# Kernel optimization log

Hardware: AMD Instinct MI355X
Metric: run time of the kernel (lower is better)

The kernel has to match this reference:

```python
import jax, jax.numpy as jnp
import numpy as np

NUM_ANCHORS = 5
NUM_CLASSES = 20


def setup_inputs() -> dict:
    key = jax.random.key(0)
    k1, k2, k3, k4 = jax.random.split(key, 4)
    N, H, W, M = 64, 52, 52, 32
    img = 1664
    x = jax.random.normal(k1, (N, NUM_ANCHORS * (5 + NUM_CLASSES), H, W), jnp.float32)
    anchors = jnp.array([[1.08, 1.19], [3.42, 4.41], [6.63, 11.38],
                         [9.42, 5.11], [16.62, 10.52]], jnp.float32)
    # valid gt boxes in xyxy pixel coords
    xy = jax.random.uniform(k2, (N, M, 2), jnp.float32) * (img * 0.8)
    wh = jax.random.uniform(k3, (N, M, 2), jnp.float32) * (img * 0.2) + 1.0
    gt_boxes = jnp.concatenate([xy, xy + wh], axis=-1)
    gt_labels = jax.random.randint(k4, (N, M), 0, NUM_CLASSES)
    return dict(x=x, anchors=anchors, gt_boxes=gt_boxes, gt_labels=gt_labels,
                img_h=img, img_w=img)


def _format_outputs(x, anchors, img_h, img_w):
    # x: [N, A*(5+C), H, W] -> (coords [N,HW,A,4] (x,y,w,h), obj [N,HW,A], scores [N,HW,A,C])
    N, _, H, W = x.shape
    A = anchors.shape[0]
    t = x.reshape(N, A, 5 + NUM_CLASSES, H, W).transpose(0, 3, 4, 1, 2)  # [N,H,W,A,5+C]
    c_x = jnp.arange(W, dtype=x.dtype) * (img_w / W)
    c_y = jnp.arange(H, dtype=x.dtype) * (img_h / H)
    b_x = jax.nn.sigmoid(t[..., 0]) + c_x[None, None, :, None]   # [N,H,W,A]
    b_y = jax.nn.sigmoid(t[..., 1]) + c_y[None, :, None, None]
    b_w = (img_w / W) * anchors[:, 0] * jnp.exp(t[..., 2])
    b_h = (img_h / H) * anchors[:, 1] * jnp.exp(t[..., 3])
    coords = jnp.stack([b_x, b_y, b_w, b_h], axis=-1).reshape(N, H * W, A, 4)
    b_o = jax.nn.sigmoid(t[..., 4]).reshape(N, H * W, A)
    scores = t[..., 5:].reshape(N, H * W, A, NUM_CLASSES)
    return coords, b_o, scores


def reference(x, anchors, gt_boxes, gt_labels, img_h, img_w):
    coords, b_o, scores = _format_outputs(x, anchors, img_h, img_w)
    # pred_boxes[..., 2:] += pred_boxes[..., :2]  (xywh -> xyxy)
    boxes = jnp.concatenate([coords[..., :2], coords[..., :2] + coords[..., 2:]], axis=-1)  # [N,HW,A,4]
    # box_iou: pred [N,HW,A,1,4] vs gt [N,1,1,M,4] -> [N,HW,A,M]
    p = boxes[..., None, :]
    g = gt_boxes[:, None, None, :, :]
    lt = jnp.maximum(p[..., :2], g[..., :2])
    rb = jnp.minimum(p[..., 2:], g[..., 2:])
    whi = jnp.clip(rb - lt, 0.0)
    inter = whi[..., 0] * whi[..., 1]
    area_p = (boxes[..., 2] - boxes[..., 0]) * (boxes[..., 3] - boxes[..., 1])
    area_g = (gt_boxes[..., 2] - gt_boxes[..., 0]) * (gt_boxes[..., 3] - gt_boxes[..., 1])
    iou = inter / (area_p[..., None] + area_g[:, None, None, :] - inter)   # [N,HW,A,M]

    cell_sel = iou.max(axis=(2, 3)) > 0.0                 # [N,HW]
    best_a = jnp.argmax(iou.max(axis=3), axis=2)          # [N,HW] best anchor per cell
    iou_best = jnp.take_along_axis(iou, best_a[..., None, None], axis=2)[:, :, 0, :]  # [N,HW,M]
    max_iou = iou_best.max(axis=-1)                       # [N,HW]
    gt_idx = jnp.argmax(iou_best, axis=-1)                # [N,HW]

    sel_box = jnp.take_along_axis(boxes, best_a[..., None, None], axis=2)[:, :, 0, :]   # [N,HW,4]
    sel_o = jnp.take_along_axis(b_o, best_a[..., None], axis=2)[:, :, 0]                # [N,HW]
    sel_sc = jnp.take_along_axis(scores, best_a[..., None, None], axis=2)[:, :, 0, :]   # [N,HW,C]
    g_box = jnp.take_along_axis(gt_boxes, gt_idx[..., None], axis=1)                    # [N,HW,4]
    g_lab = jnp.take_along_axis(gt_labels, gt_idx, axis=1)                              # [N,HW]

    m = cell_sel.astype(x.dtype)
    objectness_loss = (jnp.sum(m * (sel_o - max_iou) ** 2)
                       + 0.5 * jnp.sum((1.0 - m) * b_o.max(axis=2) ** 2))
    bbox_loss = (jnp.sum(m * jnp.sum((sel_box[..., :2] - g_box[..., :2]) ** 2, axis=-1))
                 + jnp.sum(m * jnp.sum((jnp.sqrt(sel_box[..., 2:]) - jnp.sqrt(g_box[..., 2:])) ** 2, axis=-1)))
    logp = jax.nn.log_softmax(sel_sc, axis=-1)
    ce = -jnp.take_along_axis(logp, g_lab[..., None], axis=-1)[..., 0]
    clf_loss = jnp.sum(m * ce)
    return jnp.stack([objectness_loss, bbox_loss, clf_loss])
```

## Files before the change

kernel.cpp:

```cpp
#include <hip/hip_runtime.h>
#include <math.h>

#define A_ 5
#define C_ 20
#define N_ 64
#define H_ 52
#define W_ 52
#define HW_ (H_ * W_)
#define M_ 32
#define CH_ (A_ * (5 + C_))
#define CPB 64
#define NBLK_X ((HW_ + CPB - 1) / CPB)
#define NBLK (NBLK_X * N_)

__global__ __launch_bounds__(320) void yolo_main(
    const float* __restrict__ x,
    const float* __restrict__ anchors,
    const float* __restrict__ gt,
    const int* __restrict__ glab,
    const void* img_h_p, const void* img_w_p,
    float* __restrict__ ws)
{
    __shared__ float s_c[8][A_][CPB];

    const int tid  = threadIdx.x;
    const int a    = tid >> 6;
    const int lane = tid & 63;
    const int n    = blockIdx.y;
    const int cell = blockIdx.x * CPB + lane;
    const bool valid = cell < HW_;

    int ibw = *(const int*)img_w_p;
    float img_w = (ibw > 0 && ibw < 1000000) ? (float)ibw : *(const float*)img_w_p;
    int ibh = *(const int*)img_h_p;
    float img_h = (ibh > 0 && ibh < 1000000) ? (float)ibh : *(const float*)img_h_p;
    const float sx = img_w / (float)W_;
    const float sy = img_h / (float)H_;

    const float ax = anchors[2 * a];
    const float ay = anchors[2 * a + 1];

    float bi = 0.f, bu = 1.f;
    int   bm = 0;
    float x1 = 0.f, y1 = 0.f, x2 = 0.f, y2 = 0.f, ov = 0.f;

    if (valid) {
        const int wi = cell % W_;
        const int hi = cell / W_;
        const size_t base = (size_t)n * CH_ * HW_ + (size_t)a * 25 * HW_ + cell;
        float t0 = x[base];
        float t1 = x[base + (size_t)HW_];
        float t2 = x[base + 2 * (size_t)HW_];
        float t3 = x[base + 3 * (size_t)HW_];
        float t4 = x[base + 4 * (size_t)HW_];

        float bx = 1.f / (1.f + __expf(-t0)) + (float)wi * sx;
        float by = 1.f / (1.f + __expf(-t1)) + (float)hi * sy;
        float bw = sx * ax * __expf(t2);
        float bh = sy * ay * __expf(t3);
        x1 = bx; y1 = by; x2 = bx + bw; y2 = by + bh;
        ov = 1.f / (1.f + __expf(-t4));
        float ap = (x2 - x1) * (y2 - y1);

        const float4* gtv = (const float4*)(gt + (size_t)n * M_ * 4);
        #pragma unroll 8
        for (int m = 0; m < M_; ++m) {
            float4 g = gtv[m];
            float area = (g.z - g.x) * (g.w - g.y);
            float wxi = fminf(x2, g.z) - fmaxf(x1, g.x);
            float hyi = fminf(y2, g.w) - fmaxf(y1, g.y);
            wxi = fmaxf(wxi, 0.f);
            hyi = fmaxf(hyi, 0.f);
            float inter = wxi * hyi;
            float uni = ap + area - inter;
            if (inter * bu > bi * uni) { bi = inter; bu = uni; bm = m; }
        }
    }

    s_c[0][a][lane] = bi;
    s_c[1][a][lane] = bu;
    s_c[2][a][lane] = x1;
    s_c[3][a][lane] = y1;
    s_c[4][a][lane] = x2;
    s_c[5][a][lane] = y2;
    s_c[6][a][lane] = ov;
    s_c[7][a][lane] = __int_as_float(bm);
    __syncthreads();

    if (tid < 64) {
        float obj = 0.f, bbx = 0.f, clf = 0.f;

        float Bi = 0.f, Bu = 1.f;
        int Ba = 0, Bm = 0;
        float X1 = 0.f, Y1 = 0.f, X2 = 0.f, Y2 = 0.f, O = 0.f;
        float bomax = -1e30f;
        #pragma unroll
        for (int aa = 0; aa < A_; ++aa) {
            float ci = s_c[0][aa][lane];
            float cu = s_c[1][aa][lane];
            float co = s_c[6][aa][lane];
            bomax = fmaxf(bomax, co);
            bool upd = (aa == 0) || (ci * Bu > Bi * cu);
            if (upd) {
                Bi = ci; Bu = cu; Ba = aa;
                Bm = __float_as_int(s_c[7][aa][lane]);
                X1 = s_c[2][aa][lane]; Y1 = s_c[3][aa][lane];
                X2 = s_c[4][aa][lane]; Y2 = s_c[5][aa][lane];
                O = co;
            }
        }

        if (valid) {
            if (Bi > 0.f) {
                float miou = Bi / Bu;
                float d = O - miou;
                obj = d * d;

                float4 g = ((const float4*)gt)[n * M_ + Bm];
                float d0 = X1 - g.x;
                float d1 = Y1 - g.y;
                float d2 = sqrtf(X2) - sqrtf(g.z);
                float d3 = sqrtf(Y2) - sqrtf(g.w);
                bbx = d0 * d0 + d1 * d1 + d2 * d2 + d3 * d3;

                const size_t sb = (size_t)n * CH_ * HW_ + (size_t)(Ba * 25 + 5) * HW_ + cell;
                const int lab = glab[n * M_ + Bm];
                float mx = -1e30f, se = 0.f, scl = 0.f;
                #pragma unroll
                for (int j = 0; j < C_; ++j) {
                    float v = x[sb + (size_t)j * HW_];
                    float nm = fmaxf(mx, v);
                    se = se * __expf(mx - nm) + __expf(v - nm);
                    mx = nm;
                    scl = (j == lab) ? v : scl;
                }
                clf = mx + __logf(se) - scl;
            } else {
                obj = 0.5f * bomax * bomax;
            }
        }

        #pragma unroll
        for (int off = 32; off > 0; off >>= 1) {
            obj += __shfl_down(obj, off, 64);
            bbx += __shfl_down(bbx, off, 64);
            clf += __shfl_down(clf, off, 64);
        }
        if (tid == 0) {
            const int bid = blockIdx.y * gridDim.x + blockIdx.x;
            ws[bid * 3 + 0] = obj;
            ws[bid * 3 + 1] = bbx;
            ws[bid * 3 + 2] = clf;
        }
    }
}

__global__ __launch_bounds__(256) void yolo_reduce(
    const float* __restrict__ ws, float* __restrict__ out)
{
    __shared__ float s_red[4][3];
    const int tid = threadIdx.x;
    float o = 0.f, b = 0.f, c = 0.f;
    for (int e = tid; e < NBLK; e += 256) {
        o += ws[e * 3 + 0];
        b += ws[e * 3 + 1];
        c += ws[e * 3 + 2];
    }
    #pragma unroll
    for (int off = 32; off > 0; off >>= 1) {
        o += __shfl_down(o, off, 64);
        b += __shfl_down(b, off, 64);
        c += __shfl_down(c, off, 64);
    }
    const int wid = tid >> 6;
    if ((tid & 63) == 0) {
        s_red[wid][0] = o; s_red[wid][1] = b; s_red[wid][2] = c;
    }
    __syncthreads();
    if (tid == 0) {
        float oo = 0.f, bb = 0.f, cc = 0.f;
        #pragma unroll
        for (int w = 0; w < 4; ++w) {
            oo += s_red[w][0]; bb += s_red[w][1]; cc += s_red[w][2];
        }
        out[0] = oo; out[1] = bb; out[2] = cc;
    }
}

extern "C" void kernel_launch(void* const* d_in, const int* in_sizes, int n_in,
                              void* d_out, int out_size, void* d_ws, size_t ws_size,
                              hipStream_t stream) {
    const float* x    = (const float*)d_in[0];
    const float* anch = (const float*)d_in[1];
    const float* gt   = (const float*)d_in[2];
    const int*   gl   = (const int*)d_in[3];
    const void*  ih   = d_in[4];
    const void*  iw   = d_in[5];
    float* out = (float*)d_out;
    float* ws  = (float*)d_ws;

    dim3 grid(NBLK_X, N_);
    yolo_main<<<grid, dim3(320), 0, stream>>>(x, anch, gt, gl, ih, iw, ws);
    yolo_reduce<<<1, 256, 0, stream>>>(ws, out);
}
```

Measured before the change: 141.7 us.

## Compute per-anchor CE and bbox loss upfront, removing dependent score gather

Each anchor thread now loads its 20 class logits together with its box channels and computes its own cross-entropy and bbox error against its best-matching gt box. The winner selection then just picks precomputed values from shared memory. This removes a serialized second read of class scores done by a single wavefront per block, at the cost of redundant softmax work on every anchor and more registers. The workspace partials are also switched to a struct-of-arrays layout and the final reduce uses 1024 threads.

```diff
diff --git a/kernel.cpp b/kernel.cpp
--- a/kernel.cpp
+++ b/kernel.cpp
@@ -21,7 +21,7 @@
     const void* img_h_p, const void* img_w_p,
     float* __restrict__ ws)
 {
-    __shared__ float s_c[8][A_][CPB];
+    __shared__ float s_c[5][A_][CPB];
 
     const int tid  = threadIdx.x;
     const int a    = tid >> 6;
@@ -42,7 +42,7 @@
 
     float bi = 0.f, bu = 1.f;
     int   bm = 0;
-    float x1 = 0.f, y1 = 0.f, x2 = 0.f, y2 = 0.f, ov = 0.f;
+    float ov = 0.f, ce = 0.f, bb = 0.f;
 
     if (valid) {
         const int wi = cell % W_;
@@ -53,12 +53,16 @@
         float t2 = x[base + 2 * (size_t)HW_];
         float t3 = x[base + 3 * (size_t)HW_];
         float t4 = x[base + 4 * (size_t)HW_];
+        float sc[C_];
+        #pragma unroll
+        for (int j = 0; j < C_; ++j)
+            sc[j] = x[base + (size_t)(5 + j) * HW_];
 
         float bx = 1.f / (1.f + __expf(-t0)) + (float)wi * sx;
         float by = 1.f / (1.f + __expf(-t1)) + (float)hi * sy;
         float bw = sx * ax * __expf(t2);
         float bh = sy * ay * __expf(t3);
-        x1 = bx; y1 = by; x2 = bx + bw; y2 = by + bh;
+        float x1 = bx, y1 = by, x2 = bx + bw, y2 = by + bh;
         ov = 1.f / (1.f + __expf(-t4));
         float ap = (x2 - x1) * (y2 - y1);
 
@@ -75,66 +79,58 @@
             float uni = ap + area - inter;
             if (inter * bu > bi * uni) { bi = inter; bu = uni; bm = m; }
         }
+
+        float4 g = ((const float4*)gt)[n * M_ + bm];
+        int lab = glab[n * M_ + bm];
+        float d0 = x1 - g.x;
+        float d1 = y1 - g.y;
+        float d2 = sqrtf(x2) - sqrtf(g.z);
+        float d3 = sqrtf(y2) - sqrtf(g.w);
+        bb = d0 * d0 + d1 * d1 + d2 * d2 + d3 * d3;
+
+        float mx = sc[0];
+        #pragma unroll
+        for (int j = 1; j < C_; ++j) mx = fmaxf(mx, sc[j]);
+        float se = 0.f, scl = sc[0];
+        #pragma unroll
+        for (int j = 0; j < C_; ++j) {
+            se += __expf(sc[j] - mx);
+            scl = (j == lab) ? sc[j] : scl;
+        }
+        ce = mx + __logf(se) - scl;
     }
 
     s_c[0][a][lane] = bi;
     s_c[1][a][lane] = bu;
-    s_c[2][a][lane] = x1;
-    s_c[3][a][lane] = y1;
-    s_c[4][a][lane] = x2;
-    s_c[5][a][lane] = y2;
-    s_c[6][a][lane] = ov;
-    s_c[7][a][lane] = __int_as_float(bm);
+    s_c[2][a][lane] = ov;
+    s_c[3][a][lane] = ce;
+    s_c[4][a][lane] = bb;
     __syncthreads();
 
     if (tid < 64) {
-        float obj = 0.f, bbx = 0.f, clf = 0.f;
-
-        float Bi = 0.f, Bu = 1.f;
-        int Ba = 0, Bm = 0;
-        float X1 = 0.f, Y1 = 0.f, X2 = 0.f, Y2 = 0.f, O = 0.f;
+        float Bi = 0.f, Bu = 1.f, O = 0.f, CE = 0.f, BB = 0.f;
         float bomax = -1e30f;
         #pragma unroll
         for (int aa = 0; aa < A_; ++aa) {
             float ci = s_c[0][aa][lane];
             float cu = s_c[1][aa][lane];
-            float co = s_c[6][aa][lane];
+            float co = s_c[2][aa][lane];
             bomax = fmaxf(bomax, co);
             bool upd = (aa == 0) || (ci * Bu > Bi * cu);
             if (upd) {
-                Bi = ci; Bu = cu; Ba = aa;
-                Bm = __float_as_int(s_c[7][aa][lane]);
-                X1 = s_c[2][aa][lane]; Y1 = s_c[3][aa][lane];
-                X2 = s_c[4][aa][lane]; Y2 = s_c[5][aa][lane];
-                O = co;
+                Bi = ci; Bu = cu; O = co;
+                CE = s_c[3][aa][lane];
+                BB = s_c[4][aa][lane];
             }
         }
 
+        float obj = 0.f, bbx = 0.f, clf = 0.f;
         if (valid) {
             if (Bi > 0.f) {
-                float miou = Bi / Bu;
-                float d = O - miou;
+                float d = O - Bi / Bu;
                 obj = d * d;
-
-                float4 g = ((const float4*)gt)[n * M_ + Bm];
-                float d0 = X1 - g.x;
-                float d1 = Y1 - g.y;
-                float d2 = sqrtf(X2) - sqrtf(g.z);
-                float d3 = sqrtf(Y2) - sqrtf(g.w);
-                bbx = d0 * d0 + d1 * d1 + d2 * d2 + d3 * d3;
-
-                const size_t sb = (size_t)n * CH_ * HW_ + (size_t)(Ba * 25 + 5) * HW_ + cell;
-                const int lab = glab[n * M_ + Bm];
-                float mx = -1e30f, se = 0.f, scl = 0.f;
-                #pragma unroll
-                for (int j = 0; j < C_; ++j) {
-                    float v = x[sb + (size_t)j * HW_];
-                    float nm = fmaxf(mx, v);
-                    se = se * __expf(mx - nm) + __expf(v - nm);
-                    mx = nm;
-                    scl = (j == lab) ? v : scl;
-                }
-                clf = mx + __logf(se) - scl;
+                bbx = BB;
+                clf = CE;
             } else {
                 obj = 0.5f * bomax * bomax;
             }
@@ -148,23 +144,23 @@
         }
         if (tid == 0) {
             const int bid = blockIdx.y * gridDim.x + blockIdx.x;
-            ws[bid * 3 + 0] = obj;
-            ws[bid * 3 + 1] = bbx;
-            ws[bid * 3 + 2] = clf;
+            ws[0 * NBLK + bid] = obj;
+            ws[1 * NBLK + bid] = bbx;
+            ws[2 * NBLK + bid] = clf;
         }
     }
 }
 
-__global__ __launch_bounds__(256) void yolo_reduce(
+__global__ __launch_bounds__(1024) void yolo_reduce(
     const float* __restrict__ ws, float* __restrict__ out)
 {
-    __shared__ float s_red[4][3];
+    __shared__ float s_red[16][3];
     const int tid = threadIdx.x;
     float o = 0.f, b = 0.f, c = 0.f;
-    for (int e = tid; e < NBLK; e += 256) {
-        o += ws[e * 3 + 0];
-        b += ws[e * 3 + 1];
-        c += ws[e * 3 + 2];
+    for (int e = tid; e < NBLK; e += 1024) {
+        o += ws[0 * NBLK + e];
+        b += ws[1 * NBLK + e];
+        c += ws[2 * NBLK + e];
     }
     #pragma unroll
     for (int off = 32; off > 0; off >>= 1) {
@@ -180,7 +176,7 @@
     if (tid == 0) {
         float oo = 0.f, bb = 0.f, cc = 0.f;
         #pragma unroll
-        for (int w = 0; w < 4; ++w) {
+        for (int w = 0; w < 16; ++w) {
             oo += s_red[w][0]; bb += s_red[w][1]; cc += s_red[w][2];
         }
         out[0] = oo; out[1] = bb; out[2] = cc;
@@ -190,6 +186,7 @@
 extern "C" void kernel_launch(void* const* d_in, const int* in_sizes, int n_in,
                               void* d_out, int out_size, void* d_ws, size_t ws_size,
                               hipStream_t stream) {
+    (void)in_sizes; (void)n_in; (void)out_size; (void)ws_size;
     const float* x    = (const float*)d_in[0];
     const float* anch = (const float*)d_in[1];
     const float* gt   = (const float*)d_in[2];
@@ -201,5 +198,5 @@
 
     dim3 grid(NBLK_X, N_);
     yolo_main<<<grid, dim3(320), 0, stream>>>(x, anch, gt, gl, ih, iw, ws);
-    yolo_reduce<<<1, 256, 0, stream>>>(ws, out);
+    yolo_reduce<<<1, 1024, 0, stream>>>(ws, out);
 }
```

Measured after the change: 143.3 us. About the same (+1.2%).
